# Optimization experiments

Measured on AMD Instinct MI355X. Metric: run time of the kernel, lower is better.

The kernel has to match this reference:

```python
import jax, jax.numpy as jnp
import numpy as np

B, S, NQ, FFN, EMB = 8, 4096, 8, 2048, 512


def setup_inputs() -> dict:
    key = jax.random.key(0)
    k0, k1, k2, k3 = jax.random.split(key, 4)
    x = jax.random.normal(k0, (B, S, NQ), dtype=jnp.float32)
    theta = jax.random.normal(k1, (NQ,), dtype=jnp.float32)  # trainable RY angles
    W1 = jax.random.normal(k2, (NQ, FFN), dtype=jnp.float32) / np.float32(np.sqrt(NQ))
    b1 = jnp.zeros((FFN,), dtype=jnp.float32)
    W2 = jax.random.normal(k3, (FFN, EMB), dtype=jnp.float32) / np.float32(np.sqrt(FFN))
    b2 = jnp.zeros((EMB,), dtype=jnp.float32)
    return {"x": x, "theta": theta, "W1": W1, "b1": b1, "W2": W2, "b2": b2}


def reference(x, theta, W1, b1, W2, b2):
    # Quantum layer: per wire i, state RY(theta_i) RX(x_i) |0>; no entangling gates,
    # so the state is a product state and <PauliZ_i> = cos(x_i) * cos(theta_i) exactly.
    # This fuses the per-token / per-gate simulation loop into one batched expression.
    q = jnp.cos(x) * jnp.cos(theta)                     # [B, S, NQ]
    # Dropout is identity at eval time.
    h = jax.nn.relu(jnp.einsum("bsq,qf->bsf", q, W1) + b1)  # [B, S, FFN]
    out = jnp.einsum("bsf,fe->bse", h, W2) + b2             # [B, S, EMB]
    return out
```

## Files before the change

### kernel.cpp

```cpp
#include <hip/hip_runtime.h>

#define T_TOK 32768
#define NQ    8
#define FFN   2048
#define EMB   512
#define BM    128
#define BN    128
#define BK    64
#define NCHUNK (FFN / BK)
#define HPAD  72

typedef __attribute__((ext_vector_type(8))) short  short8;
typedef __attribute__((ext_vector_type(4))) float  float4v;

__device__ __forceinline__ unsigned short f2bf(float f) {
  unsigned int u = __float_as_uint(f);
  u += 0x7fffu + ((u >> 16) & 1u);
  return (unsigned short)(u >> 16);
}

__device__ __forceinline__ unsigned pk2bf(float lo, float hi) {
#if __has_builtin(__builtin_amdgcn_cvt_pk_bf16_f32)
  typedef __attribute__((ext_vector_type(2))) __bf16 bf2;
  bf2 p = __builtin_amdgcn_cvt_pk_bf16_f32(lo, hi);
  return *(unsigned*)&p;
#else
  return (unsigned)f2bf(lo) | ((unsigned)f2bf(hi) << 16);
#endif
}

__global__ void prep_all(const float* __restrict__ W1,
                         const float* __restrict__ W2,
                         unsigned short* __restrict__ w1t,
                         unsigned short* __restrict__ w2t) {
  __shared__ float t[32][33];
  const int kb = blockIdx.x * 32;
  const int nb = blockIdx.y * 32;
  const int c = threadIdx.x & 31, r0 = threadIdx.x >> 5;
#pragma unroll
  for (int p = 0; p < 4; ++p) {
    int r = r0 + p * 8;
    t[r][c] = W2[(size_t)(kb + r) * EMB + nb + c];
  }
  __syncthreads();
#pragma unroll
  for (int p = 0; p < 4; ++p) {
    int r = r0 + p * 8;
    w2t[(size_t)(nb + r) * FFN + kb + c] = f2bf(t[c][r]);
  }
  if (blockIdx.x == 0) {
    const int base = blockIdx.y * 1024 + threadIdx.x * 4;
#pragma unroll
    for (int e = 0; e < 4; ++e) {
      int idx = base + e;
      int f = idx >> 3, i = idx & 7;
      w1t[idx] = f2bf(W1[i * FFN + f]);
    }
  }
}

__global__ __launch_bounds__(256, 4) void ffq_main(
    const float* __restrict__ x,
    const float* __restrict__ theta,
    const unsigned short* __restrict__ w1t,
    const float* __restrict__ b1,
    const unsigned short* __restrict__ w2t,
    const float* __restrict__ b2,
    float* __restrict__ out) {

  __shared__ unsigned short h_lds[BM][HPAD];
  __shared__ unsigned short w2_lds[BN * BK];

  const int tid  = threadIdx.x;
  const int wave = tid >> 6;
  const int lane = tid & 63;
  const int l15  = lane & 15;
  const int quad = lane >> 4;
  const int tok0 = blockIdx.x * BM;
  const int n0   = blockIdx.y * BN;
  const int wr   = wave >> 1;
  const int wc   = wave & 1;

  float cth[8];
  {
    const float4* tp = (const float4*)theta;
    float4 t0 = tp[0], t1 = tp[1];
    cth[0] = __cosf(t0.x); cth[1] = __cosf(t0.y);
    cth[2] = __cosf(t0.z); cth[3] = __cosf(t0.w);
    cth[4] = __cosf(t1.x); cth[5] = __cosf(t1.y);
    cth[6] = __cosf(t1.z); cth[7] = __cosf(t1.w);
  }
  short8 bq[2];
#pragma unroll
  for (int g = 0; g < 2; ++g) {
    short8 v = (short8){0,0,0,0,0,0,0,0};
    if (lane < 16) {
      int tok = tok0 + 32 * wave + 16 * g + lane;
      const float4* xp = (const float4*)(x + (size_t)tok * NQ);
      float4 x0 = xp[0], x1 = xp[1];
      float q0 = __cosf(x0.x) * cth[0], q1 = __cosf(x0.y) * cth[1];
      float q2 = __cosf(x0.z) * cth[2], q3 = __cosf(x0.w) * cth[3];
      float q4 = __cosf(x1.x) * cth[4], q5 = __cosf(x1.y) * cth[5];
      float q6 = __cosf(x1.z) * cth[6], q7 = __cosf(x1.w) * cth[7];
      uint4 uu;
      uu.x = pk2bf(q0, q1); uu.y = pk2bf(q2, q3);
      uu.z = pk2bf(q4, q5); uu.w = pk2bf(q6, q7);
      v = *(short8*)&uu;
    }
    bq[g] = v;
  }

  float4v acc[4][4];
#pragma unroll
  for (int i = 0; i < 4; ++i)
#pragma unroll
    for (int j = 0; j < 4; ++j)
      acc[i][j] = (float4v){0.f, 0.f, 0.f, 0.f};

  for (int kc = 0; kc < NCHUNK; ++kc) {
    const int k0 = kc * BK;

    __syncthreads();

    short8 aw[4];
    float4 bias[4];
#pragma unroll
    for (int kt = 0; kt < 4; ++kt) {
      aw[kt]   = *(const short8*)(w1t + (size_t)(k0 + kt * 16 + l15) * NQ);
      bias[kt] = *(const float4*)(b1 + k0 + kt * 16 + quad * 4);
    }

    {
      const int r = tid >> 3;
      const int c = tid & 7;
#pragma unroll
      for (int issue = 0; issue < 4; ++issue) {
        const int row    = issue * 32 + r;
        const int gchunk = c ^ (row & 7);
        const unsigned short* g =
            w2t + (size_t)(n0 + row) * FFN + k0 + gchunk * 8;
        unsigned short* l = &w2_lds[issue * 2048 + tid * 8];
        __builtin_amdgcn_global_load_lds(
            (const __attribute__((address_space(1))) void*)g,
            (__attribute__((address_space(3))) void*)l, 16, 0, 0);
      }
    }

#pragma unroll
    for (int kt = 0; kt < 4; ++kt) {
      float4v c0 = (float4v){0.f, 0.f, 0.f, 0.f};
      float4v c1 = (float4v){0.f, 0.f, 0.f, 0.f};
      c0 = __builtin_amdgcn_mfma_f32_16x16x32_bf16(aw[kt], bq[0], c0, 0, 0, 0);
      c1 = __builtin_amdgcn_mfma_f32_16x16x32_bf16(aw[kt], bq[1], c1, 0, 0, 0);
      float v0[4], v1[4];
#pragma unroll
      for (int r = 0; r < 4; ++r) {
        float a0 = c0[r] + bias[kt][r]; v0[r] = a0 > 0.f ? a0 : 0.f;
        float a1 = c1[r] + bias[kt][r]; v1[r] = a1 > 0.f ? a1 : 0.f;
      }
      uint2 p0, p1;
      p0.x = pk2bf(v0[0], v0[1]); p0.y = pk2bf(v0[2], v0[3]);
      p1.x = pk2bf(v1[0], v1[1]); p1.y = pk2bf(v1[2], v1[3]);
      *((uint2*)&h_lds[32 * wave + l15][kt * 16 + quad * 4])      = p0;
      *((uint2*)&h_lds[32 * wave + 16 + l15][kt * 16 + quad * 4]) = p1;
    }

    __syncthreads();

#pragma unroll
    for (int ks = 0; ks < 2; ++ks) {
      short8 af[4], bf[4];
#pragma unroll
      for (int mt = 0; mt < 4; ++mt)
        af[mt] = *(const short8*)&h_lds[wr * 64 + mt * 16 + l15]
                                       [ks * 32 + quad * 8];
#pragma unroll
      for (int nt = 0; nt < 4; ++nt) {
        const int n  = wc * 64 + nt * 16 + l15;
        const int sc = (ks * 4 + quad) ^ (n & 7);
        bf[nt] = *(const short8*)&w2_lds[n * BK + sc * 8];
      }
#pragma unroll
      for (int mt = 0; mt < 4; ++mt)
#pragma unroll
        for (int nt = 0; nt < 4; ++nt)
          acc[mt][nt] = __builtin_amdgcn_mfma_f32_16x16x32_bf16(
              af[mt], bf[nt], acc[mt][nt], 0, 0, 0);
    }
  }

#pragma unroll
  for (int nt = 0; nt < 4; ++nt) {
    const int col = n0 + wc * 64 + nt * 16 + l15;
    const float bv = b2[col];
#pragma unroll
    for (int mt = 0; mt < 4; ++mt) {
      const int row0 = tok0 + wr * 64 + mt * 16 + quad * 4;
#pragma unroll
      for (int r = 0; r < 4; ++r) {
        out[(size_t)(row0 + r) * EMB + col] = acc[mt][nt][r] + bv;
      }
    }
  }
}

extern "C" void kernel_launch(void* const* d_in, const int* in_sizes, int n_in,
                              void* d_out, int out_size, void* d_ws, size_t ws_size,
                              hipStream_t stream) {
  const float* x     = (const float*)d_in[0];
  const float* theta = (const float*)d_in[1];
  const float* W1    = (const float*)d_in[2];
  const float* b1    = (const float*)d_in[3];
  const float* W2    = (const float*)d_in[4];
  const float* b2    = (const float*)d_in[5];
  float* out = (float*)d_out;

  unsigned short* w1t = (unsigned short*)d_ws;
  unsigned short* w2t = w1t + FFN * NQ;

  prep_all<<<dim3(FFN / 32, EMB / 32), 256, 0, stream>>>(W1, W2, w1t, w2t);

  dim3 grid(T_TOK / BM, EMB / BN);
  ffq_main<<<grid, 256, 0, stream>>>(x, theta, w1t, b1, w2t, b2, out);
}
```

Measured before the change: 176.0 us.

## Double-buffer W2 and W1/bias chunks in LDS with next-chunk prefetch

Adds ping-pong LDS buffers for the W2 tile and for the W1/b1 slices. The next K-chunk is issued with global_load_lds while the current chunk is being computed, so global load latency overlaps the MFMA work. The two __syncthreads per chunk become raw s_barrier calls with hand-placed s_waitcnt vmcnt counts, and the h stores are moved after the barrier. The extra LDS lowers the launch-bounds occupancy target from 4 to 3 blocks per CU, trading latency hiding through occupancy for explicit software pipelining.

```diff
diff --git a/kernel.cpp b/kernel.cpp
--- a/kernel.cpp
+++ b/kernel.cpp
@@ -59,7 +59,7 @@
   }
 }
 
-__global__ __launch_bounds__(256, 4) void ffq_main(
+__global__ __launch_bounds__(256, 3) void ffq_main(
     const float* __restrict__ x,
     const float* __restrict__ theta,
     const unsigned short* __restrict__ w1t,
@@ -68,8 +68,10 @@
     const float* __restrict__ b2,
     float* __restrict__ out) {
 
-  __shared__ unsigned short h_lds[BM][HPAD];
-  __shared__ unsigned short w2_lds[BN * BK];
+  __shared__ __align__(16) unsigned short h_lds[BM][HPAD];
+  __shared__ __align__(16) unsigned short w2_lds[2][BN * BK];
+  __shared__ __align__(16) unsigned short w1_lds[2][BK * NQ];
+  __shared__ __align__(16) float          b1_lds[2][BK];
 
   const int tid  = threadIdx.x;
   const int wave = tid >> 6;
@@ -110,6 +112,33 @@
     bq[g] = v;
   }
 
+  const int sw_r = tid >> 3;
+  const int sw_c = tid & 7;
+
+  auto stage_w1b1 = [&](int kc_, int b_) {
+    const int k0_ = kc_ * BK;
+    __builtin_amdgcn_global_load_lds(
+        (const __attribute__((address_space(1))) void*)(w1t + (size_t)(k0_ + lane) * NQ),
+        (__attribute__((address_space(3))) void*)(&w1_lds[b_][lane * NQ]), 16, 0, 0);
+    __builtin_amdgcn_global_load_lds(
+        (const __attribute__((address_space(1))) void*)(b1 + k0_ + lane),
+        (__attribute__((address_space(3))) void*)(&b1_lds[b_][lane]), 4, 0, 0);
+  };
+
+  auto stage_w2 = [&](int kc_, int b_) {
+    const int k0_ = kc_ * BK;
+#pragma unroll
+    for (int issue = 0; issue < 4; ++issue) {
+      const int row    = issue * 32 + sw_r;
+      const int gchunk = sw_c ^ (row & 7);
+      __builtin_amdgcn_global_load_lds(
+          (const __attribute__((address_space(1))) void*)(
+              w2t + (size_t)(n0 + row) * FFN + k0_ + gchunk * 8),
+          (__attribute__((address_space(3))) void*)(&w2_lds[b_][issue * 2048 + tid * 8]),
+          16, 0, 0);
+    }
+  };
+
   float4v acc[4][4];
 #pragma unroll
   for (int i = 0; i < 4; ++i)
@@ -117,35 +146,28 @@
     for (int j = 0; j < 4; ++j)
       acc[i][j] = (float4v){0.f, 0.f, 0.f, 0.f};
 
+  stage_w1b1(0, 0);
+  stage_w2(0, 0);
+  asm volatile("s_waitcnt vmcnt(4)" ::: "memory");
+  __builtin_amdgcn_s_barrier();
+  __builtin_amdgcn_sched_barrier(0);
+
   for (int kc = 0; kc < NCHUNK; ++kc) {
-    const int k0 = kc * BK;
-
-    __syncthreads();
+    const int buf  = kc & 1;
+    const int nbuf = buf ^ 1;
+    const int nc   = (kc + 1 < NCHUNK) ? (kc + 1) : (NCHUNK - 1);
 
     short8 aw[4];
     float4 bias[4];
 #pragma unroll
     for (int kt = 0; kt < 4; ++kt) {
-      aw[kt]   = *(const short8*)(w1t + (size_t)(k0 + kt * 16 + l15) * NQ);
-      bias[kt] = *(const float4*)(b1 + k0 + kt * 16 + quad * 4);
-    }
-
-    {
-      const int r = tid >> 3;
-      const int c = tid & 7;
-#pragma unroll
-      for (int issue = 0; issue < 4; ++issue) {
-        const int row    = issue * 32 + r;
-        const int gchunk = c ^ (row & 7);
-        const unsigned short* g =
-            w2t + (size_t)(n0 + row) * FFN + k0 + gchunk * 8;
-        unsigned short* l = &w2_lds[issue * 2048 + tid * 8];
-        __builtin_amdgcn_global_load_lds(
-            (const __attribute__((address_space(1))) void*)g,
-            (__attribute__((address_space(3))) void*)l, 16, 0, 0);
-      }
-    }
-
+      aw[kt]   = *(const short8*)&w1_lds[buf][(kt * 16 + l15) * NQ];
+      bias[kt] = *(const float4*)&b1_lds[buf][kt * 16 + quad * 4];
+    }
+
+    stage_w1b1(nc, nbuf);
+
+    uint2 p0[4], p1[4];
 #pragma unroll
     for (int kt = 0; kt < 4; ++kt) {
       float4v c0 = (float4v){0.f, 0.f, 0.f, 0.f};
@@ -158,14 +180,24 @@
         float a0 = c0[r] + bias[kt][r]; v0[r] = a0 > 0.f ? a0 : 0.f;
         float a1 = c1[r] + bias[kt][r]; v1[r] = a1 > 0.f ? a1 : 0.f;
       }
-      uint2 p0, p1;
-      p0.x = pk2bf(v0[0], v0[1]); p0.y = pk2bf(v0[2], v0[3]);
-      p1.x = pk2bf(v1[0], v1[1]); p1.y = pk2bf(v1[2], v1[3]);
-      *((uint2*)&h_lds[32 * wave + l15][kt * 16 + quad * 4])      = p0;
-      *((uint2*)&h_lds[32 * wave + 16 + l15][kt * 16 + quad * 4]) = p1;
-    }
-
-    __syncthreads();
+      p0[kt].x = pk2bf(v0[0], v0[1]); p0[kt].y = pk2bf(v0[2], v0[3]);
+      p1[kt].x = pk2bf(v1[0], v1[1]); p1[kt].y = pk2bf(v1[2], v1[3]);
+    }
+
+    __builtin_amdgcn_s_barrier();
+    __builtin_amdgcn_sched_barrier(0);
+
+    stage_w2(nc, nbuf);
+
+#pragma unroll
+    for (int kt = 0; kt < 4; ++kt) {
+      *((uint2*)&h_lds[32 * wave + l15][kt * 16 + quad * 4])      = p0[kt];
+      *((uint2*)&h_lds[32 * wave + 16 + l15][kt * 16 + quad * 4]) = p1[kt];
+    }
+
+    asm volatile("s_waitcnt vmcnt(4) lgkmcnt(0)" ::: "memory");
+    __builtin_amdgcn_s_barrier();
+    __builtin_amdgcn_sched_barrier(0);
 
 #pragma unroll
     for (int ks = 0; ks < 2; ++ks) {
@@ -178,7 +210,7 @@
       for (int nt = 0; nt < 4; ++nt) {
         const int n  = wc * 64 + nt * 16 + l15;
         const int sc = (ks * 4 + quad) ^ (n & 7);
-        bf[nt] = *(const short8*)&w2_lds[n * BK + sc * 8];
+        bf[nt] = *(const short8*)&w2_lds[buf][n * BK + sc * 8];
       }
 #pragma unroll
       for (int mt = 0; mt < 4; ++mt)
@@ -188,6 +220,8 @@
               af[mt], bf[nt], acc[mt][nt], 0, 0, 0);
     }
   }
+
+  asm volatile("s_waitcnt vmcnt(0)" ::: "memory");
 
 #pragma unroll
   for (int nt = 0; nt < 4; ++nt) {
```

Result: slower. 182.8 us (+3.9%).

## Double-buffer W2 tiles and give each wave private h rows to drop a barrier

Applied to the files above, without the earlier changes.

Halves the K chunk to 32 and double-buffers the W2 LDS tile, prefetching the next chunk with global_load_lds while the current one is consumed. Each wave now owns its 32 tokens and computes all 128 output columns, so the h tile is written and read only by that wave. This removes the second block-wide barrier per chunk and uses a new padded h layout and a new swizzle. It also adds sched_barrier and setprio hints around the MFMA phase. The cost is twice as many loop iterations, each with a barrier, and W2 fragments that are no longer shared across waves in registers.

```diff
diff --git a/kernel.cpp b/kernel.cpp
--- a/kernel.cpp
+++ b/kernel.cpp
@@ -6,9 +6,9 @@
 #define EMB   512
 #define BM    128
 #define BN    128
-#define BK    64
+#define BK    32
 #define NCHUNK (FFN / BK)
-#define HPAD  72
+#define HROW  36
 
 typedef __attribute__((ext_vector_type(8))) short  short8;
 typedef __attribute__((ext_vector_type(4))) float  float4v;
@@ -29,6 +29,13 @@
 #endif
 }
 
+__device__ __forceinline__ short8 ld_h8(const unsigned short* p) {
+  uint2 a = *(const uint2*)p;
+  uint2 b = *(const uint2*)(p + 4);
+  uint4 u; u.x = a.x; u.y = a.y; u.z = b.x; u.w = b.y;
+  return *(short8*)&u;
+}
+
 __global__ void prep_all(const float* __restrict__ W1,
                          const float* __restrict__ W2,
                          unsigned short* __restrict__ w1t,
@@ -68,8 +75,8 @@
     const float* __restrict__ b2,
     float* __restrict__ out) {
 
-  __shared__ unsigned short h_lds[BM][HPAD];
-  __shared__ unsigned short w2_lds[BN * BK];
+  __shared__ __align__(16) unsigned short w2_lds[2][BN * BK];
+  __shared__ __align__(16) unsigned short h_lds[4][32 * HROW];
 
   const int tid  = threadIdx.x;
   const int wave = tid >> 6;
@@ -78,8 +85,8 @@
   const int quad = lane >> 4;
   const int tok0 = blockIdx.x * BM;
   const int n0   = blockIdx.y * BN;
-  const int wr   = wave >> 1;
-  const int wc   = wave & 1;
+
+  unsigned short* hb = &h_lds[wave][0];
 
   float cth[8];
   {
@@ -110,92 +117,114 @@
     bq[g] = v;
   }
 
-  float4v acc[4][4];
-#pragma unroll
-  for (int i = 0; i < 4; ++i)
-#pragma unroll
-    for (int j = 0; j < 4; ++j)
+  const int st_row = tid >> 2;
+  const int st_gc  = (tid & 3) ^ ((tid >> 3) & 3);
+
+  auto stage_w2 = [&](int kc_, int b_) {
+    const int k0_ = kc_ * BK;
+#pragma unroll
+    for (int issue = 0; issue < 2; ++issue) {
+      const int r = issue * 64 + st_row;
+      __builtin_amdgcn_global_load_lds(
+          (const __attribute__((address_space(1))) void*)(
+              w2t + (size_t)(n0 + r) * FFN + k0_ + st_gc * 8),
+          (__attribute__((address_space(3))) void*)(
+              &w2_lds[b_][issue * 2048 + tid * 8]),
+          16, 0, 0);
+    }
+  };
+
+  float4v acc[2][8];
+#pragma unroll
+  for (int i = 0; i < 2; ++i)
+#pragma unroll
+    for (int j = 0; j < 8; ++j)
       acc[i][j] = (float4v){0.f, 0.f, 0.f, 0.f};
 
+  const int bf_c    = quad ^ ((l15 >> 1) & 3);
+  const unsigned short* w2r[2] = {
+      &w2_lds[0][l15 * BK + bf_c * 8],
+      &w2_lds[1][l15 * BK + bf_c * 8]};
+  unsigned short* hw0 = hb + l15 * HROW + quad * 4;
+  unsigned short* hw1 = hb + (16 + l15) * HROW + quad * 4;
+  const unsigned short* hr0 = hb + l15 * HROW + quad * 8;
+  const unsigned short* hr1 = hb + (16 + l15) * HROW + quad * 8;
+
+  stage_w2(0, 0);
+
+#pragma unroll 2
   for (int kc = 0; kc < NCHUNK; ++kc) {
-    const int k0 = kc * BK;
-
-    __syncthreads();
-
-    short8 aw[4];
-    float4 bias[4];
-#pragma unroll
-    for (int kt = 0; kt < 4; ++kt) {
-      aw[kt]   = *(const short8*)(w1t + (size_t)(k0 + kt * 16 + l15) * NQ);
-      bias[kt] = *(const float4*)(b1 + k0 + kt * 16 + quad * 4);
-    }
+    const int buf = kc & 1;
+    const int k0  = kc * BK;
+    const int nc  = (kc + 1 < NCHUNK) ? kc + 1 : NCHUNK - 1;
+    asm volatile("s_waitcnt vmcnt(0)" ::: "memory");
+    __builtin_amdgcn_s_barrier();
+    __builtin_amdgcn_sched_barrier(0);
+
+    short8 aw0 = *(const short8*)(w1t + (size_t)(k0 + l15) * NQ);
+    short8 aw1 = *(const short8*)(w1t + (size_t)(k0 + 16 + l15) * NQ);
+    float4 bi0 = *(const float4*)(b1 + k0 + quad * 4);
+    float4 bi1 = *(const float4*)(b1 + k0 + 16 + quad * 4);
+    __builtin_amdgcn_sched_barrier(0);
+
+    stage_w2(nc, buf ^ 1);
+    __builtin_amdgcn_sched_barrier(0);
 
     {
-      const int r = tid >> 3;
-      const int c = tid & 7;
-#pragma unroll
-      for (int issue = 0; issue < 4; ++issue) {
-        const int row    = issue * 32 + r;
-        const int gchunk = c ^ (row & 7);
-        const unsigned short* g =
-            w2t + (size_t)(n0 + row) * FFN + k0 + gchunk * 8;
-        unsigned short* l = &w2_lds[issue * 2048 + tid * 8];
-        __builtin_amdgcn_global_load_lds(
-            (const __attribute__((address_space(1))) void*)g,
-            (__attribute__((address_space(3))) void*)l, 16, 0, 0);
+      float4v c00 = (float4v){0.f,0.f,0.f,0.f}, c01 = c00, c10 = c00, c11 = c00;
+      c00 = __builtin_amdgcn_mfma_f32_16x16x32_bf16(aw0, bq[0], c00, 0, 0, 0);
+      c01 = __builtin_amdgcn_mfma_f32_16x16x32_bf16(aw0, bq[1], c01, 0, 0, 0);
+      c10 = __builtin_amdgcn_mfma_f32_16x16x32_bf16(aw1, bq[0], c10, 0, 0, 0);
+      c11 = __builtin_amdgcn_mfma_f32_16x16x32_bf16(aw1, bq[1], c11, 0, 0, 0);
+      float v00[4], v01[4], v10[4], v11[4];
+#pragma unroll
+      for (int r = 0; r < 4; ++r) {
+        float a;
+        a = c00[r] + bi0[r]; v00[r] = a > 0.f ? a : 0.f;
+        a = c01[r] + bi0[r]; v01[r] = a > 0.f ? a : 0.f;
+        a = c10[r] + bi1[r]; v10[r] = a > 0.f ? a : 0.f;
+        a = c11[r] + bi1[r]; v11[r] = a > 0.f ? a : 0.f;
       }
-    }
-
-#pragma unroll
-    for (int kt = 0; kt < 4; ++kt) {
-      float4v c0 = (float4v){0.f, 0.f, 0.f, 0.f};
-      float4v c1 = (float4v){0.f, 0.f, 0.f, 0.f};
-      c0 = __builtin_amdgcn_mfma_f32_16x16x32_bf16(aw[kt], bq[0], c0, 0, 0, 0);
-      c1 = __builtin_amdgcn_mfma_f32_16x16x32_bf16(aw[kt], bq[1], c1, 0, 0, 0);
-      float v0[4], v1[4];
-#pragma unroll
-      for (int r = 0; r < 4; ++r) {
-        float a0 = c0[r] + bias[kt][r]; v0[r] = a0 > 0.f ? a0 : 0.f;
-        float a1 = c1[r] + bias[kt][r]; v1[r] = a1 > 0.f ? a1 : 0.f;
+      uint2 p;
+      p.x = pk2bf(v00[0], v00[1]); p.y = pk2bf(v00[2], v00[3]);
+      *(uint2*)(hw0)      = p;
+      p.x = pk2bf(v01[0], v01[1]); p.y = pk2bf(v01[2], v01[3]);
+      *(uint2*)(hw1)      = p;
+      p.x = pk2bf(v10[0], v10[1]); p.y = pk2bf(v10[2], v10[3]);
+      *(uint2*)(hw0 + 16) = p;
+      p.x = pk2bf(v11[0], v11[1]); p.y = pk2bf(v11[2], v11[3]);
+      *(uint2*)(hw1 + 16) = p;
+    }
+
+    asm volatile("s_waitcnt lgkmcnt(0)" ::: "memory");
+    __builtin_amdgcn_sched_barrier(0);
+
+    __builtin_amdgcn_s_setprio(1);
+    {
+      short8 af0 = ld_h8(hr0);
+      short8 af1 = ld_h8(hr1);
+      const unsigned short* wb = w2r[buf];
+#pragma unroll
+      for (int nt = 0; nt < 8; ++nt) {
+        short8 bf = *(const short8*)(wb + nt * 512);
+        acc[0][nt] = __builtin_amdgcn_mfma_f32_16x16x32_bf16(
+            af0, bf, acc[0][nt], 0, 0, 0);
+        acc[1][nt] = __builtin_amdgcn_mfma_f32_16x16x32_bf16(
+            af1, bf, acc[1][nt], 0, 0, 0);
       }
-      uint2 p0, p1;
-      p0.x = pk2bf(v0[0], v0[1]); p0.y = pk2bf(v0[2], v0[3]);
-      p1.x = pk2bf(v1[0], v1[1]); p1.y = pk2bf(v1[2], v1[3]);
-      *((uint2*)&h_lds[32 * wave + l15][kt * 16 + quad * 4])      = p0;
-      *((uint2*)&h_lds[32 * wave + 16 + l15][kt * 16 + quad * 4]) = p1;
-    }
-
-    __syncthreads();
-
-#pragma unroll
-    for (int ks = 0; ks < 2; ++ks) {
-      short8 af[4], bf[4];
-#pragma unroll
-      for (int mt = 0; mt < 4; ++mt)
-        af[mt] = *(const short8*)&h_lds[wr * 64 + mt * 16 + l15]
-                                       [ks * 32 + quad * 8];
-#pragma unroll
-      for (int nt = 0; nt < 4; ++nt) {
-        const int n  = wc * 64 + nt * 16 + l15;
-        const int sc = (ks * 4 + quad) ^ (n & 7);
-        bf[nt] = *(const short8*)&w2_lds[n * BK + sc * 8];
-      }
-#pragma unroll
-      for (int mt = 0; mt < 4; ++mt)
-#pragma unroll
-        for (int nt = 0; nt < 4; ++nt)
-          acc[mt][nt] = __builtin_amdgcn_mfma_f32_16x16x32_bf16(
-              af[mt], bf[nt], acc[mt][nt], 0, 0, 0);
-    }
-  }
-
-#pragma unroll
-  for (int nt = 0; nt < 4; ++nt) {
-    const int col = n0 + wc * 64 + nt * 16 + l15;
+    }
+    __builtin_amdgcn_s_setprio(0);
+  }
+
+  asm volatile("s_waitcnt vmcnt(0)" ::: "memory");
+
+#pragma unroll
+  for (int nt = 0; nt < 8; ++nt) {
+    const int col = n0 + nt * 16 + l15;
     const float bv = b2[col];
 #pragma unroll
-    for (int mt = 0; mt < 4; ++mt) {
-      const int row0 = tok0 + wr * 64 + mt * 16 + quad * 4;
+    for (int mt = 0; mt < 2; ++mt) {
+      const int row0 = tok0 + wave * 32 + mt * 16 + quad * 4;
 #pragma unroll
       for (int r = 0; r < 4; ++r) {
         out[(size_t)(row0 + r) * EMB + col] = acc[mt][nt][r] + bv;
```

Measured after the change: 171.6 us. 1.03x faster.
